# Kernel tuning notes

Hardware: AMD Instinct MI355X
Metric: run time of the kernel (lower is better)

The kernel has to match this reference:

```python
import jax, jax.numpy as jnp
import numpy as np

B, N, T, F_IN, U = 8192, 8, 12, 16, 64
H = U // 2


def setup_inputs():
    key = jax.random.key(0)
    ks = jax.random.split(key, 30)
    def w(k, shape, s=0.08):
        return jax.random.normal(k, shape, jnp.float32) * s
    return {
        "ts": jax.random.normal(ks[0], (B, T, F_IN), jnp.float32),
        "gts": jax.random.normal(ks[1], (B, N, T, F_IN), jnp.float32),
        "emb_w": w(ks[2], (H, F_IN)), "emb_b": w(ks[3], (H,)),
        "attQ_w": w(ks[4], (U, U)), "attQ_b": w(ks[5], (U,)),
        "attK_w": w(ks[6], (U, U)), "attK_b": w(ks[7], (U,)),
        "attV_w": w(ks[8], (U, U)), "attV_b": w(ks[9], (U,)),
        "attF_w": w(ks[10], (U, 2 * U)), "attF_b": w(ks[11], (U,)),
        "fuse1_w": w(ks[12], (U, 2 * U)), "fuse1_b": w(ks[13], (U,)),
        "enc_Wih": w(ks[14], (T, 4 * U, H)), "enc_Whh": w(ks[15], (T, 4 * U, U)),
        "enc_bih": w(ks[16], (T, 4 * U)), "enc_bhh": w(ks[17], (T, 4 * U)),
        "enc2_Wih": w(ks[18], (N, T, 4 * U, H)), "enc2_Whh": w(ks[19], (N, T, 4 * U, U)),
        "enc2_bih": w(ks[20], (N, T, 4 * U)), "enc2_bhh": w(ks[21], (N, T, 4 * U)),
        "mlp1_w": w(ks[22], (H, U)), "mlp1_b": w(ks[23], (H,)),
        "mlp2_w": w(ks[24], (1, H)), "mlp2_b": w(ks[25], (1,)),
    }


def _lstm(x, h, c, Wih, Whh, bih, bhh):
    # torch.nn.LSTMCell gate order: i, f, g, o
    g = x @ Wih.T + h @ Whh.T + bih + bhh
    i, f, gg, o = jnp.split(g, 4, axis=-1)
    c2 = jax.nn.sigmoid(f) * c + jax.nn.sigmoid(i) * jnp.tanh(gg)
    return jax.nn.sigmoid(o) * jnp.tanh(c2), c2


def _lstm_nodes(x, h, c, Wih, Whh, bih, bhh):
    # x: (B,N,in), h/c: (B,N,U), Wih: (N,4U,in), Whh: (N,4U,U) -- distinct cell per node
    g = (jnp.einsum('bni,nji->bnj', x, Wih)
         + jnp.einsum('bnh,njh->bnj', h, Whh)
         + bih[None] + bhh[None])
    i, f, gg, o = jnp.split(g, 4, axis=-1)
    c2 = jax.nn.sigmoid(f) * c + jax.nn.sigmoid(i) * jnp.tanh(gg)
    return jax.nn.sigmoid(o) * jnp.tanh(c2), c2


def _att(query, keys, Qw, Qb, Kw, Kb, Vw, Vb, Fw, Fb):
    # batched version of ATT.forward(norm=False): per-key scores -> softmax over keys
    q = query @ Qw.T + Qb                    # (B,U)
    k = keys @ Kw.T + Kb                     # (B,N,U)
    v = keys @ Vw.T + Vb                     # (B,N,U)
    p = jax.nn.softmax(jnp.einsum('bu,bnu->bn', q, k) / jnp.sqrt(jnp.float32(U)), axis=-1)
    ctx = jnp.einsum('bn,bnu->bu', p, v)
    return jax.nn.relu(jnp.concatenate([ctx, query], axis=-1) @ Fw.T + Fb)


def _forward(ts, gts, emb_w, emb_b, attQ_w, attQ_b, attK_w, attK_b, attV_w, attV_b,
             attF_w, attF_b, fuse1_w, fuse1_b, enc_Wih, enc_Whh, enc_bih, enc_bhh,
             enc2_Wih, enc2_Whh, enc2_bih, enc2_bhh, mlp1_w, mlp1_b, mlp2_w, mlp2_b):
    b = ts.shape[0]
    ts_e = ts @ emb_w.T + emb_b              # (B,T,H)
    gts_e = gts @ emb_w.T + emb_b            # (B,N,T,H)
    z = jnp.zeros((b, U), ts.dtype)
    zn = jnp.zeros((b, N, U), ts.dtype)

    # step 0: zero initial state; the original discards step-0 cell state (c reset to zeros)
    h_ts, _ = _lstm(ts_e[:, 0], z, z, enc_Wih[0], enc_Whh[0], enc_bih[0], enc_bhh[0])
    h_g, _ = _lstm_nodes(gts_e[:, :, 0], zn, zn, enc2_Wih[:, 0], enc2_Whh[:, 0], enc2_bih[:, 0], enc2_bhh[:, 0])
    h_ts_a = _att(h_ts, h_g, attQ_w, attQ_b, attK_w, attK_b, attV_w, attV_b, attF_w, attF_b)
    h_rep = jnp.broadcast_to(h_ts[:, None, :], h_g.shape)
    h_gts = jax.nn.relu(jnp.concatenate([h_g, h_rep], axis=-1) @ fuse1_w.T + fuse1_b)

    def step(carry, xs):
        h_ts, c_ts, h_ts_a, h_gts, c_gts = carry
        x_ts, x_g, Wih, Whh, bih, bhh, W2ih, W2hh, b2ih, b2hh = xs
        h_ts, c_ts = _lstm(x_ts, h_ts_a, c_ts, Wih, Whh, bih, bhh)
        h_g, c_gts = _lstm_nodes(x_g, h_gts, c_gts, W2ih, W2hh, b2ih, b2hh)
        h_ts_a = _att(h_ts, h_g, attQ_w, attQ_b, attK_w, attK_b, attV_w, attV_b, attF_w, attF_b)
        h_rep = jnp.broadcast_to(h_ts[:, None, :], h_g.shape)
        h_gts = jax.nn.relu(jnp.concatenate([h_g, h_rep], axis=-1) @ fuse1_w.T + fuse1_b)
        return (h_ts, c_ts, h_ts_a, h_gts, c_gts), None

    xs = (
        jnp.swapaxes(ts_e[:, 1:], 0, 1),                 # (T-1,B,H)
        jnp.transpose(gts_e[:, :, 1:], (2, 0, 1, 3)),     # (T-1,B,N,H)
        enc_Wih[1:], enc_Whh[1:], enc_bih[1:], enc_bhh[1:],
        jnp.swapaxes(enc2_Wih, 0, 1)[1:], jnp.swapaxes(enc2_Whh, 0, 1)[1:],
        jnp.swapaxes(enc2_bih, 0, 1)[1:], jnp.swapaxes(enc2_bhh, 0, 1)[1:],
    )
    carry = (h_ts, z, h_ts_a, h_gts, zn)
    (h_ts, c_ts, h_ts_a, h_gts, c_gts), _ = jax.lax.scan(step, carry, xs)

    # mlp (eval mode: dropout is identity): Linear -> ReLU -> Linear
    hid = jax.nn.relu(h_ts_a @ mlp1_w.T + mlp1_b)
    return hid @ mlp2_w.T + mlp2_b            # (B,1)


def reference(ts, gts, emb_w, emb_b, attQ_w, attQ_b, attK_w, attK_b, attV_w, attV_b,
              attF_w, attF_b, fuse1_w, fuse1_b, enc_Wih, enc_Whh, enc_bih, enc_bhh,
              enc2_Wih, enc2_Whh, enc2_bih, enc2_bhh, mlp1_w, mlp1_b, mlp2_w, mlp2_b):
    return _forward(ts, gts, emb_w, emb_b, attQ_w, attQ_b, attK_w, attK_b, attV_w, attV_b,
                    attF_w, attF_b, fuse1_w, fuse1_b, enc_Wih, enc_Whh, enc_bih, enc_bhh,
                    enc2_Wih, enc2_Whh, enc2_bih, enc2_bhh, mlp1_w, mlp1_b, mlp2_w, mlp2_b)
```

## Files before the change

### kernel.cpp

```cpp
#include <hip/hip_runtime.h>

#define T_SZ 12
#define R_WG 16
#define NTHR 512
#define NWG  512

typedef float  vf4 __attribute__((ext_vector_type(4)));
typedef int    vi4 __attribute__((ext_vector_type(4)));
typedef __bf16 vbf8 __attribute__((ext_vector_type(8)));

__device__ __forceinline__ float sigm(float x){ return 1.f/(1.f+__expf(-x)); }
__device__ __forceinline__ float tanh_f(float x){
  float e=__expf(2.f*x); return 1.f - 2.f/(e+1.f);
}
__device__ __forceinline__ unsigned short bf_hi(float f){
  unsigned int b=__float_as_uint(f);
  return (unsigned short)((b + 0x7fffu + ((b>>16)&1u))>>16);
}
__device__ __forceinline__ float bf_f(unsigned short h){
  return __uint_as_float(((unsigned int)h)<<16);
}
__device__ __forceinline__ vf4 mfma16(vi4 a, vi4 b, vf4 c){
  return __builtin_amdgcn_mfma_f32_16x16x32_bf16(
      __builtin_bit_cast(vbf8,a), __builtin_bit_cast(vbf8,b), c, 0, 0, 0);
}
__device__ __forceinline__ vi4 g16(const char* p){ return *(const vi4*)p; }

__device__ __forceinline__ void a_read(const char* h9,int slot,int ks,int arow,int kb,vi4& Ah,vi4& Al){
  int blk=((ks<<2)+kb)^(arow&7);
  const char* p=h9+slot*4096+(arow*8+blk)*16;
  Ah=*(const vi4*)p; Al=*(const vi4*)(p+2048);
}
__device__ __forceinline__ void h9_w1(char* h9,int slot,int row,int k,float v){
  int off=slot*4096+(row*8+((k>>3)^(row&7)))*16+(k&7)*2;
  unsigned short hi=bf_hi(v);
  *(unsigned short*)(h9+off)=hi;
  *(unsigned short*)(h9+off+2048)=bf_hi(v-bf_f(hi));
}
__device__ __forceinline__ void h9_w2(char* h9,int slot,int row,int k0,float v0,float v1){
  int off=slot*4096+(row*8+((k0>>3)^(row&7)))*16+(k0&7)*2;
  unsigned short h0=bf_hi(v0),h1=bf_hi(v1);
  *(unsigned*)(h9+off)=(unsigned)h0|((unsigned)h1<<16);
  *(unsigned*)(h9+off+2048)=(unsigned)bf_hi(v0-bf_f(h0))|((unsigned)bf_hi(v1-bf_f(h1))<<16);
}
__device__ __forceinline__ void h9_w4c(char* h9,int slot,int row,int k0,vf4 v){
  int off=slot*4096+(row*8+((k0>>3)^(row&7)))*16+(k0&7)*2;
  unsigned short h0=bf_hi(v[0]),h1=bf_hi(v[1]),h2=bf_hi(v[2]),h3=bf_hi(v[3]);
  uint2 hv; hv.x=(unsigned)h0|((unsigned)h1<<16); hv.y=(unsigned)h2|((unsigned)h3<<16);
  *(uint2*)(h9+off)=hv;
  uint2 lv;
  lv.x=(unsigned)bf_hi(v[0]-bf_f(h0))|((unsigned)bf_hi(v[1]-bf_f(h1))<<16);
  lv.y=(unsigned)bf_hi(v[2]-bf_f(h2))|((unsigned)bf_hi(v[3]-bf_f(h3))<<16);
  *(uint2*)(h9+off+2048)=lv;
}
__device__ __forceinline__ float h9_rd(const char* h9,int slot,int row,int k){
  int off=slot*4096+(row*8+((k>>3)^(row&7)))*16+(k&7)*2;
  return bf_f(*(const unsigned short*)(h9+off))+bf_f(*(const unsigned short*)(h9+off+2048));
}

struct Ptrs {
  const unsigned short* Wm; const unsigned short* Wa; const unsigned short* Xf;
  const float* Fbp; const float* bqk; const float* f1b;
  const float* m1w; const float* m1b; const float* m2w; const float* m2b;
  float* out;
};

__global__ __launch_bounds__(NTHR,4) void fused_kernel(Ptrs P){
  __shared__ __align__(16) char  h9[77824];
  __shared__ __align__(16) float pbuf[128];

  const int tid=threadIdx.x;
  const int r0=blockIdx.x*R_WG;
  const int w=tid>>6, ln=tid&63;
  const bool w4=(w<4);
  const int arow=ln&15, kb=ln>>4;
  const int rowL=ln&15;
  const int uA=((2*w)>>2)*16 + (ln>>4)*4 + ((2*w)&3);
  const int ub=(w&3)*16 + (ln>>4)*4;
  const char* Wmb=(const char*)P.Wm;
  const char* Wab=(const char*)P.Wa;
  const char* Xfb=(const char*)P.Xf + (size_t)(r0+arow)*9*24*32;
  float* qkf=(float*)(h9+10*4096);
  const int b0=((2*w+0)*64+ln)*16, b1=((2*w+1)*64+ln)*16;
  const int ab0=(((w&3)*4+0)*64+ln)*16, ab1=(((w&3)*4+1)*64+ln)*16;
  const int ab2=(((w&3)*4+2)*64+ln)*16, ab3=(((w&3)*4+3)*64+ln)*16;

  const vf4 bqk4=*(const vf4*)(P.bqk+ub);
  const vf4 bF4 =*(const vf4*)(P.Fbp+ub);
  const vf4 bf14=*(const vf4*)(P.f1b+ub);

  float cst[9][2];
  #pragma unroll
  for(int l=0;l<9;l++){ cst[l][0]=0.f; cst[l][1]=0.f; }

  for(int i=tid;i<77824/16;i+=NTHR) ((vi4*)h9)[i]=(vi4){0,0,0,0};
  __syncthreads();

  auto attn_gemm=[&](const char* Wc,int slot,vf4 acc)->vf4{
    vi4 Bh,Bl;
    vi4 W0=g16(Wc+ab0),W1=g16(Wc+ab1),W2=g16(Wc+ab2),W3=g16(Wc+ab3);
    a_read(h9,slot,0,arow,kb,Bh,Bl);
    acc=mfma16(W0,Bh,acc); acc=mfma16(W0,Bl,acc); acc=mfma16(W1,Bh,acc);
    a_read(h9,slot,1,arow,kb,Bh,Bl);
    acc=mfma16(W2,Bh,acc); acc=mfma16(W2,Bl,acc); acc=mfma16(W3,Bh,acc);
    return acc;
  };

  for(int t=0;t<T_SZ;t++){
    #pragma unroll
    for(int l=0;l<9;l++){
      const int slotA=(l==0)?0:l;
      const int slotW=(l==0)?9:(10+l);
      const char* Wl=Wmb + ((size_t)(l*12+t)*6)*16384;
      vf4 a0={0,0,0,0},a1={0,0,0,0};
      vi4 Bh,Bl,Wh0,Wh1,Wl0,Wl1;
      Wh0=g16(Wl+b0); Wh1=g16(Wl+b1); Wl0=g16(Wl+16384+b0); Wl1=g16(Wl+16384+b1);
      a_read(h9,slotA,0,arow,kb,Bh,Bl);
      a0=mfma16(Wh0,Bh,a0); a0=mfma16(Wh0,Bl,a0); a0=mfma16(Wl0,Bh,a0);
      a1=mfma16(Wh1,Bh,a1); a1=mfma16(Wh1,Bl,a1); a1=mfma16(Wl1,Bh,a1);
      Wh0=g16(Wl+2*16384+b0); Wh1=g16(Wl+2*16384+b1);
      Wl0=g16(Wl+3*16384+b0); Wl1=g16(Wl+3*16384+b1);
      a_read(h9,slotA,1,arow,kb,Bh,Bl);
      a0=mfma16(Wh0,Bh,a0); a0=mfma16(Wh0,Bl,a0); a0=mfma16(Wl0,Bh,a0);
      a1=mfma16(Wh1,Bh,a1); a1=mfma16(Wh1,Bl,a1); a1=mfma16(Wl1,Bh,a1);
      Wh0=g16(Wl+4*16384+b0); Wh1=g16(Wl+4*16384+b1);
      Wl0=g16(Wl+5*16384+b0); Wl1=g16(Wl+5*16384+b1);
      if(kb<2){
        const char* xp=Xfb + (size_t)(l*24 + t*2 + kb)*32;
        Bh=g16(xp); Bl=g16(xp+16);
      } else if(kb==2){ Bh=(vi4){0x3F80,0,0,0}; Bl=(vi4){0,0,0,0}; }
      else            { Bh=(vi4){0,0,0,0};     Bl=(vi4){0,0,0,0}; }
      a0=mfma16(Wh0,Bh,a0); a0=mfma16(Wh0,Bl,a0); a0=mfma16(Wl0,Bh,a0);
      a1=mfma16(Wh1,Bh,a1); a1=mfma16(Wh1,Bl,a1); a1=mfma16(Wl1,Bh,a1);
      {
        float iv=sigm(a0[0]), fv=sigm(a0[1]), gv=tanh_f(a0[2]), ov=sigm(a0[3]);
        float c20=fv*cst[l][0]+iv*gv;
        cst[l][0]=c20;
        float h0v=ov*tanh_f(c20);
        iv=sigm(a1[0]); fv=sigm(a1[1]); gv=tanh_f(a1[2]); ov=sigm(a1[3]);
        float c21=fv*cst[l][1]+iv*gv;
        cst[l][1]=c21;
        float h1v=ov*tanh_f(c21);
        h9_w2(h9,slotW,rowL,uA,h0v,h1v);
      }
      __syncthreads();
    }

    const bool dofuse=(t<T_SZ-1);
    vf4 g1,g2,g3,g4,g5,g6,g7,g8;
    if(w4){
      vf4 aq=attn_gemm(Wab+0*16384, 9, bqk4);
      *(vf4*)(qkf + rowL*64 + ub) = aq;
    } else if(dofuse){
      vf4 facc=attn_gemm(Wab+3*16384, 9, bf14);
      const char* Wc=Wab+4*16384;
      vi4 W0=g16(Wc+ab0),W1=g16(Wc+ab1),W2=g16(Wc+ab2),W3=g16(Wc+ab3);
      vi4 Bh,Bl;
      g1=facc;g2=facc;g3=facc;g4=facc;g5=facc;g6=facc;g7=facc;g8=facc;
      #define FUSE(gn,slot) \
        a_read(h9,slot,0,arow,kb,Bh,Bl); \
        gn=mfma16(W0,Bh,gn); gn=mfma16(W0,Bl,gn); gn=mfma16(W1,Bh,gn); \
        a_read(h9,slot,1,arow,kb,Bh,Bl); \
        gn=mfma16(W2,Bh,gn); gn=mfma16(W2,Bl,gn); gn=mfma16(W3,Bh,gn);
      FUSE(g1,11) FUSE(g2,12) FUSE(g3,13) FUSE(g4,14)
      FUSE(g5,15) FUSE(g6,16) FUSE(g7,17) FUSE(g8,18)
      #undef FUSE
    }
    __syncthreads();
    if(tid<128){
      int rr=tid>>3, nn=tid&7;
      const char* hp=h9+(11+nn)*4096;
      float s=0.f;
      #pragma unroll
      for(int kbl=0;kbl<8;kbl++){
        int blk=kbl^(rr&7);
        const char* pp=hp+(rr*8+blk)*16;
        vi4 hv=*(const vi4*)pp;
        vi4 lv=*(const vi4*)(pp+2048);
        const float* qkp=qkf+rr*64+kbl*8;
        #pragma unroll
        for(int e=0;e<4;e++){
          unsigned hw=((const unsigned*)&hv)[e], lw=((const unsigned*)&lv)[e];
          float w0=__uint_as_float(hw<<16)+__uint_as_float(lw<<16);
          float w1=__uint_as_float(hw&0xffff0000u)+__uint_as_float(lw&0xffff0000u);
          s+=w0*qkp[e*2]+w1*qkp[e*2+1];
        }
      }
      float mx=s;
      mx=fmaxf(mx,__shfl_xor(mx,1));
      mx=fmaxf(mx,__shfl_xor(mx,2));
      mx=fmaxf(mx,__shfl_xor(mx,4));
      float e=__expf(s-mx);
      float sm=e;
      sm+=__shfl_xor(sm,1); sm+=__shfl_xor(sm,2); sm+=__shfl_xor(sm,4);
      pbuf[tid]=e/sm;
    }
    __syncthreads();
    {
      #pragma unroll
      for(int ri=0;ri<2;ri++){
        int row=w*2+ri;
        float sa=0.f;
        #pragma unroll
        for(int n=0;n<8;n++) sa+=pbuf[row*8+n]*h9_rd(h9,11+n,row,ln);
        h9_w1(h9,10,row,ln,sa);
      }
    }
    __syncthreads();
    if(w4){
      vf4 acA=attn_gemm(Wab+1*16384, 10, bF4);
      acA=attn_gemm(Wab+2*16384, 9, acA);
      acA[0]=fmaxf(acA[0],0.f); acA[1]=fmaxf(acA[1],0.f);
      acA[2]=fmaxf(acA[2],0.f); acA[3]=fmaxf(acA[3],0.f);
      h9_w4c(h9,0,rowL,ub,acA);
    } else if(dofuse){
      #define WRX(gn,slot) \
        gn[0]=fmaxf(gn[0],0.f); gn[1]=fmaxf(gn[1],0.f); \
        gn[2]=fmaxf(gn[2],0.f); gn[3]=fmaxf(gn[3],0.f); \
        h9_w4c(h9,slot,rowL,ub,gn);
      WRX(g1,1) WRX(g2,2) WRX(g3,3) WRX(g4,4)
      WRX(g5,5) WRX(g6,6) WRX(g7,7) WRX(g8,8)
      #undef WRX
    }
    __syncthreads();
  }

  {
    float* hid=(float*)(h9+10*4096);
    int rr=tid>>5, ii=tid&31;
    float h=P.m1b[ii];
    for(int k=0;k<64;k++) h+=h9_rd(h9,0,rr,k)*P.m1w[(size_t)ii*64+k];
    hid[rr*32+ii]=fmaxf(h,0.f);
    __syncthreads();
    if(tid<R_WG){
      float s=P.m2b[0];
      for(int i=0;i<32;i++) s+=hid[tid*32+i]*P.m2w[i];
      P.out[r0+tid]=s;
    }
  }
}

__global__ void prep_wm(const float* eW, const float* eU, const float* e2W, const float* e2U,
                        const float* emb_w, const float* eb_ih, const float* eb_hh,
                        const float* e2b_ih, const float* e2b_hh, const float* emb_b,
                        unsigned short* dst){
  int id=blockIdx.x*256+threadIdx.x;
  if(id>=108*3*16*64) return;
  int lane=id&63;
  int q=id>>6;
  int wnt=q&15;
  int q2=q>>4;
  int ks=q2%3;
  int lt=q2/3;
  int LL=lt/12, t=lt%12;
  int c15=lane&15;
  int u=(wnt>>2)*16+(c15>>2)*4+(wnt&3);
  int gt=c15&3;
  int jg=gt*64+u;
  const float* Whh=(LL==0)? eU+((size_t)t*256+jg)*64 : e2U+(((size_t)(LL-1)*12+t)*256+jg)*64;
  const float* Wih=(LL==0)? eW+((size_t)t*256+jg)*32 : e2W+(((size_t)(LL-1)*12+t)*256+jg)*32;
  float bsum;
  {
    float bi=(LL==0)? eb_ih[t*256+jg] : e2b_ih[((LL-1)*12+t)*256+jg];
    float bh=(LL==0)? eb_hh[t*256+jg] : e2b_hh[((LL-1)*12+t)*256+jg];
    float s=bi+bh;
    for(int i=0;i<32;i++) s+=Wih[i]*emb_b[i];
    bsum=s;
  }
  #pragma unroll
  for(int j=0;j<8;j++){
    int k=ks*32+(lane>>4)*8+j;
    float v;
    if(k<64) v=Whh[k];
    else if(k<80){
      int kx=k-64; float s=0.f;
      for(int i=0;i<32;i++) s+=Wih[i]*emb_w[i*16+kx];
      v=s;
    } else if(k==80) v=bsum;
    else v=0.f;
    unsigned short hi=bf_hi(v), lo=bf_hi(v-bf_f(hi));
    size_t base=((size_t)lt*6+ks*2)*8192 + ((size_t)wnt*64+lane)*8 + j;
    dst[base]=hi;
    dst[base+8192]=lo;
  }
}

__global__ void prep_attw(const float* Qw, const float* Qb, const float* Kw,
                          const float* Vw, const float* Vb,
                          const float* Fw, const float* Fb, const float* f1w,
                          unsigned short* dst, float* Fbp, float* bqk){
  int id=blockIdx.x*256+threadIdx.x;
  if(id<5120){
    int cidx=id>>10;
    int rem=id&1023;
    int block=rem>>6;
    int lane=rem&63;
    int ks=(block>>1)&1, s=block&1;
    int col=(block>>2)*16+(lane&15);
    #pragma unroll
    for(int j=0;j<8;j++){
      int k=ks*32+(lane>>4)*8+j;
      float v;
      if(cidx==0){ float sv=0.f; for(int m=0;m<64;m++) sv+=Qw[m*64+k]*Kw[m*64+col]; v=sv*0.125f; }
      else if(cidx==1){ float sv=0.f; for(int m=0;m<64;m++) sv+=Fw[col*128+m]*Vw[m*64+k]; v=sv; }
      else if(cidx==2) v=Fw[col*128+64+k];
      else if(cidx==3) v=f1w[col*128+64+k];
      else             v=f1w[col*128+k];
      unsigned short hi=bf_hi(v);
      dst[(size_t)cidx*8192 + ((size_t)block*64+lane)*8 + j] = (s==0)? hi : bf_hi(v-bf_f(hi));
    }
  } else if(id<5184){
    int u=id-5120;
    float s=Fb[u];
    for(int m=0;m<64;m++) s+=Fw[u*128+m]*Vb[m];
    Fbp[u]=s;
  } else if(id<5248){
    int m=id-5184;
    float s=0.f;
    for(int u=0;u<64;u++) s+=Qb[u]*Kw[u*64+m];
    bqk[m]=s*0.125f;
  }
}

__global__ void prep_xf(const float* ts, const float* gts, unsigned short* xf){
  int id=blockIdx.x*256+threadIdx.x;
  if(id>=8192*9*24) return;
  int kb=id&1;
  int t=(id>>1)%12;
  int q=id/24;
  int src=q%9;
  int b=q/9;
  const float* s=(src==0)? ts+(size_t)b*192+(size_t)t*16+kb*8
                         : gts+(size_t)b*1536+(size_t)(src-1)*192+(size_t)t*16+kb*8;
  unsigned short* d=xf+(size_t)id*16;
  #pragma unroll
  for(int j=0;j<8;j++){
    float f=s[j];
    unsigned short hi=bf_hi(f);
    d[j]=hi;
    d[8+j]=bf_hi(f-bf_f(hi));
  }
}

extern "C" void kernel_launch(void* const* d_in, const int* in_sizes, int n_in,
                              void* d_out, int out_size, void* d_ws, size_t ws_size,
                              hipStream_t stream){
  const float* ts      =(const float*)d_in[0];
  const float* gts     =(const float*)d_in[1];
  const float* emb_w   =(const float*)d_in[2];
  const float* emb_b   =(const float*)d_in[3];
  const float* attQ_w  =(const float*)d_in[4];
  const float* attQ_b  =(const float*)d_in[5];
  const float* attK_w  =(const float*)d_in[6];
  const float* attV_w  =(const float*)d_in[8];
  const float* attV_b  =(const float*)d_in[9];
  const float* attF_w  =(const float*)d_in[10];
  const float* attF_b  =(const float*)d_in[11];
  const float* fuse1_w =(const float*)d_in[12];
  const float* fuse1_b =(const float*)d_in[13];
  const float* enc_Wih =(const float*)d_in[14];
  const float* enc_Whh =(const float*)d_in[15];
  const float* enc_bih =(const float*)d_in[16];
  const float* enc_bhh =(const float*)d_in[17];
  const float* enc2_Wih=(const float*)d_in[18];
  const float* enc2_Whh=(const float*)d_in[19];
  const float* enc2_bih=(const float*)d_in[20];
  const float* enc2_bhh=(const float*)d_in[21];
  const float* mlp1_w  =(const float*)d_in[22];
  const float* mlp1_b  =(const float*)d_in[23];
  const float* mlp2_w  =(const float*)d_in[24];
  const float* mlp2_b  =(const float*)d_in[25];

  char* ws=(char*)d_ws;
  size_t off=0;
  unsigned short* Wm=(unsigned short*)(ws+off); off+=(size_t)108*6*8192*2;
  unsigned short* Wa=(unsigned short*)(ws+off); off+=(size_t)5*8192*2;
  float* Fbp=(float*)(ws+off); off+=64*4;
  float* bqk=(float*)(ws+off); off+=64*4;
  unsigned short* Xf=(unsigned short*)(ws+off); off+=(size_t)8192*9*24*16*2;

  prep_wm<<<(108*3*16*64+255)/256,256,0,stream>>>(enc_Wih,enc_Whh,enc2_Wih,enc2_Whh,emb_w,
                                                  enc_bih,enc_bhh,enc2_bih,enc2_bhh,emb_b,Wm);
  prep_attw<<<21,256,0,stream>>>(attQ_w,attQ_b,attK_w,attV_w,attV_b,attF_w,attF_b,fuse1_w,
                                 Wa,Fbp,bqk);
  prep_xf<<<(8192*9*24+255)/256,256,0,stream>>>(ts,gts,Xf);

  Ptrs P;
  P.Wm=Wm; P.Wa=Wa; P.Xf=Xf;
  P.Fbp=Fbp; P.bqk=bqk; P.f1b=fuse1_b;
  P.m1w=mlp1_w; P.m1b=mlp1_b; P.m2w=mlp2_w; P.m2b=mlp2_b;
  P.out=(float*)d_out;

  fused_kernel<<<NWG,NTHR,0,stream>>>(P);
}
```

Before: 501.9 us.

## Repack LSTM and attention weights per wave and spread score dot-products across all threads

The prep kernels now write the bf16 hi/lo weight fragments so that each wave's fragments sit contiguously, 12KB per wave per LSTM cell and 4KB per wave per attention matrix. The fused kernel then addresses them with a single base pointer plus small constant offsets, which makes its global loads more local and cuts address arithmetic. The attention-score stage now uses all 512 threads, four per row-node pair with a shuffle reduction, instead of 128 threads, and reads the query-key vector as vf4. The cost is extra cross-lane shuffles and a duplicated softmax across each group of four lanes.

```diff
diff --git a/kernel.cpp b/kernel.cpp
--- a/kernel.cpp
+++ b/kernel.cpp
@@ -78,12 +78,9 @@
   const int uA=((2*w)>>2)*16 + (ln>>4)*4 + ((2*w)&3);
   const int ub=(w&3)*16 + (ln>>4)*4;
   const char* Wmb=(const char*)P.Wm;
-  const char* Wab=(const char*)P.Wa;
+  const char* awb=(const char*)P.Wa + ((size_t)(w&3))*4096 + (size_t)ln*16;
   const char* Xfb=(const char*)P.Xf + (size_t)(r0+arow)*9*24*32;
   float* qkf=(float*)(h9+10*4096);
-  const int b0=((2*w+0)*64+ln)*16, b1=((2*w+1)*64+ln)*16;
-  const int ab0=(((w&3)*4+0)*64+ln)*16, ab1=(((w&3)*4+1)*64+ln)*16;
-  const int ab2=(((w&3)*4+2)*64+ln)*16, ab3=(((w&3)*4+3)*64+ln)*16;
 
   const vf4 bqk4=*(const vf4*)(P.bqk+ub);
   const vf4 bF4 =*(const vf4*)(P.Fbp+ub);
@@ -96,9 +93,10 @@
   for(int i=tid;i<77824/16;i+=NTHR) ((vi4*)h9)[i]=(vi4){0,0,0,0};
   __syncthreads();
 
-  auto attn_gemm=[&](const char* Wc,int slot,vf4 acc)->vf4{
+  auto attn_gemm=[&](int cidx,int slot,vf4 acc)->vf4{
+    const char* Wc=awb + (size_t)cidx*16384;
     vi4 Bh,Bl;
-    vi4 W0=g16(Wc+ab0),W1=g16(Wc+ab1),W2=g16(Wc+ab2),W3=g16(Wc+ab3);
+    vi4 W0=g16(Wc),W1=g16(Wc+1024),W2=g16(Wc+2048),W3=g16(Wc+3072);
     a_read(h9,slot,0,arow,kb,Bh,Bl);
     acc=mfma16(W0,Bh,acc); acc=mfma16(W0,Bl,acc); acc=mfma16(W1,Bh,acc);
     a_read(h9,slot,1,arow,kb,Bh,Bl);
@@ -111,20 +109,24 @@
     for(int l=0;l<9;l++){
       const int slotA=(l==0)?0:l;
       const int slotW=(l==0)?9:(10+l);
-      const char* Wl=Wmb + ((size_t)(l*12+t)*6)*16384;
+      const char* Wl=Wmb + (((size_t)(l*12+t)*8 + w)*12288) + (size_t)ln*16;
       vf4 a0={0,0,0,0},a1={0,0,0,0};
       vi4 Bh,Bl,Wh0,Wh1,Wl0,Wl1;
-      Wh0=g16(Wl+b0); Wh1=g16(Wl+b1); Wl0=g16(Wl+16384+b0); Wl1=g16(Wl+16384+b1);
+      Wh0=g16(Wl); Wh1=g16(Wl+1024); Wl0=g16(Wl+2048); Wl1=g16(Wl+3072);
       a_read(h9,slotA,0,arow,kb,Bh,Bl);
       a0=mfma16(Wh0,Bh,a0); a0=mfma16(Wh0,Bl,a0); a0=mfma16(Wl0,Bh,a0);
       a1=mfma16(Wh1,Bh,a1); a1=mfma16(Wh1,Bl,a1); a1=mfma16(Wl1,Bh,a1);
-      Wh0=g16(Wl+2*16384+b0); Wh1=g16(Wl+2*16384+b1);
-      Wl0=g16(Wl+3*16384+b0); Wl1=g16(Wl+3*16384+b1);
+      {
+        const char* Wk=Wl+4096;
+        Wh0=g16(Wk); Wh1=g16(Wk+1024); Wl0=g16(Wk+2048); Wl1=g16(Wk+3072);
+      }
       a_read(h9,slotA,1,arow,kb,Bh,Bl);
       a0=mfma16(Wh0,Bh,a0); a0=mfma16(Wh0,Bl,a0); a0=mfma16(Wl0,Bh,a0);
       a1=mfma16(Wh1,Bh,a1); a1=mfma16(Wh1,Bl,a1); a1=mfma16(Wl1,Bh,a1);
-      Wh0=g16(Wl+4*16384+b0); Wh1=g16(Wl+4*16384+b1);
-      Wl0=g16(Wl+5*16384+b0); Wl1=g16(Wl+5*16384+b1);
+      {
+        const char* Wk=Wl+8192;
+        Wh0=g16(Wk); Wh1=g16(Wk+1024); Wl0=g16(Wk+2048); Wl1=g16(Wk+3072);
+      }
       if(kb<2){
         const char* xp=Xfb + (size_t)(l*24 + t*2 + kb)*32;
         Bh=g16(xp); Bl=g16(xp+16);
@@ -149,12 +151,12 @@
     const bool dofuse=(t<T_SZ-1);
     vf4 g1,g2,g3,g4,g5,g6,g7,g8;
     if(w4){
-      vf4 aq=attn_gemm(Wab+0*16384, 9, bqk4);
+      vf4 aq=attn_gemm(0, 9, bqk4);
       *(vf4*)(qkf + rowL*64 + ub) = aq;
     } else if(dofuse){
-      vf4 facc=attn_gemm(Wab+3*16384, 9, bf14);
-      const char* Wc=Wab+4*16384;
-      vi4 W0=g16(Wc+ab0),W1=g16(Wc+ab1),W2=g16(Wc+ab2),W3=g16(Wc+ab3);
+      vf4 facc=attn_gemm(3, 9, bf14);
+      const char* Wc=awb + (size_t)4*16384;
+      vi4 W0=g16(Wc),W1=g16(Wc+1024),W2=g16(Wc+2048),W3=g16(Wc+3072);
       vi4 Bh,Bl;
       g1=facc;g2=facc;g3=facc;g4=facc;g5=facc;g6=facc;g7=facc;g8=facc;
       #define FUSE(gn,slot) \
@@ -167,33 +169,39 @@
       #undef FUSE
     }
     __syncthreads();
-    if(tid<128){
-      int rr=tid>>3, nn=tid&7;
+    {
+      const int sub=tid&3, pair=tid>>2;
+      const int rr=pair>>3, nn=pair&7;
       const char* hp=h9+(11+nn)*4096;
       float s=0.f;
       #pragma unroll
-      for(int kbl=0;kbl<8;kbl++){
+      for(int ii=0;ii<2;ii++){
+        int kbl=sub*2+ii;
         int blk=kbl^(rr&7);
         const char* pp=hp+(rr*8+blk)*16;
         vi4 hv=*(const vi4*)pp;
         vi4 lv=*(const vi4*)(pp+2048);
-        const float* qkp=qkf+rr*64+kbl*8;
+        const vf4* qkp=(const vf4*)(qkf+rr*64+kbl*8);
+        vf4 q0=qkp[0], q1=qkp[1];
         #pragma unroll
         for(int e=0;e<4;e++){
           unsigned hw=((const unsigned*)&hv)[e], lw=((const unsigned*)&lv)[e];
           float w0=__uint_as_float(hw<<16)+__uint_as_float(lw<<16);
           float w1=__uint_as_float(hw&0xffff0000u)+__uint_as_float(lw&0xffff0000u);
-          s+=w0*qkp[e*2]+w1*qkp[e*2+1];
+          float qa=(e<2)? q0[e*2] : q1[(e-2)*2];
+          float qb=(e<2)? q0[e*2+1] : q1[(e-2)*2+1];
+          s+=w0*qa+w1*qb;
         }
       }
+      s+=__shfl_xor(s,1); s+=__shfl_xor(s,2);
       float mx=s;
-      mx=fmaxf(mx,__shfl_xor(mx,1));
-      mx=fmaxf(mx,__shfl_xor(mx,2));
       mx=fmaxf(mx,__shfl_xor(mx,4));
+      mx=fmaxf(mx,__shfl_xor(mx,8));
+      mx=fmaxf(mx,__shfl_xor(mx,16));
       float e=__expf(s-mx);
       float sm=e;
-      sm+=__shfl_xor(sm,1); sm+=__shfl_xor(sm,2); sm+=__shfl_xor(sm,4);
-      pbuf[tid]=e/sm;
+      sm+=__shfl_xor(sm,4); sm+=__shfl_xor(sm,8); sm+=__shfl_xor(sm,16);
+      if(sub==0) pbuf[pair]=e/sm;
     }
     __syncthreads();
     {
@@ -208,8 +216,8 @@
     }
     __syncthreads();
     if(w4){
-      vf4 acA=attn_gemm(Wab+1*16384, 10, bF4);
-      acA=attn_gemm(Wab+2*16384, 9, acA);
+      vf4 acA=attn_gemm(1, 10, bF4);
+      acA=attn_gemm(2, 9, acA);
       acA[0]=fmaxf(acA[0],0.f); acA[1]=fmaxf(acA[1],0.f);
       acA[2]=fmaxf(acA[2],0.f); acA[3]=fmaxf(acA[3],0.f);
       h9_w4c(h9,0,rowL,ub,acA);
@@ -267,6 +275,9 @@
     for(int i=0;i<32;i++) s+=Wih[i]*emb_b[i];
     bsum=s;
   }
+  int wv=wnt>>1, p=wnt&1;
+  size_t base_hi=(((size_t)lt*8+wv)*12 + (4*ks+p  ))*512 + (size_t)lane*8;
+  size_t base_lo=(((size_t)lt*8+wv)*12 + (4*ks+2+p))*512 + (size_t)lane*8;
   #pragma unroll
   for(int j=0;j<8;j++){
     int k=ks*32+(lane>>4)*8+j;
@@ -279,9 +290,8 @@
     } else if(k==80) v=bsum;
     else v=0.f;
     unsigned short hi=bf_hi(v), lo=bf_hi(v-bf_f(hi));
-    size_t base=((size_t)lt*6+ks*2)*8192 + ((size_t)wnt*64+lane)*8 + j;
-    dst[base]=hi;
-    dst[base+8192]=lo;
+    dst[base_hi+j]=hi;
+    dst[base_lo+j]=lo;
   }
 }
 
@@ -296,7 +306,10 @@
     int block=rem>>6;
     int lane=rem&63;
     int ks=(block>>1)&1, s=block&1;
-    int col=(block>>2)*16+(lane&15);
+    int cb=block>>2;
+    int qq=(ks<<1)|s;
+    int col=cb*16+(lane&15);
+    size_t base=(((size_t)cidx*4+cb)*4 + qq)*512 + (size_t)lane*8;
     #pragma unroll
     for(int j=0;j<8;j++){
       int k=ks*32+(lane>>4)*8+j;
@@ -307,7 +320,7 @@
       else if(cidx==3) v=f1w[col*128+64+k];
       else             v=f1w[col*128+k];
       unsigned short hi=bf_hi(v);
-      dst[(size_t)cidx*8192 + ((size_t)block*64+lane)*8 + j] = (s==0)? hi : bf_hi(v-bf_f(hi));
+      dst[base+j] = (s==0)? hi : bf_hi(v-bf_f(hi));
     }
   } else if(id<5184){
     int u=id-5120;
```

Result: faster. 442.4 us (-11.9%).
